# Performance work log

Hardware: AMD Instinct MI355X
Metric: run time of the kernel (lower is better)

## Reference

```python
import jax, jax.numpy as jnp
import numpy as np

N = 20000        # nodes
E = 320000       # edges (before self-loops)
V = 5000         # vocab size for each of the 5 categorical fields
L = 20           # padded token list length per node
SF = 16          # scalar feature count
ED = 32          # embedding_dim
HC = 128         # hidden_channels
NH = 4           # num_heads (conv1)
B = 8            # graphs in batch
DIN = SF + 5 * ED  # 176


def setup_inputs() -> dict:
    key = jax.random.key(0)
    ks = jax.random.split(key, 24)
    inp = {
        "x_scalar": jax.random.normal(ks[0], (N, SF), jnp.float32),
        "x_opcode": jax.random.randint(ks[1], (N, L), 0, V),
        "x_source": jax.random.randint(ks[2], (N, L), 0, V),
        "x_sink": jax.random.randint(ks[3], (N, L), 0, V),
        "x_string_manip": jax.random.randint(ks[4], (N, L), 0, V),
        "x_payload": jax.random.randint(ks[5], (N, L), 0, V),
        "edge_index": jax.random.randint(ks[6], (2, E), 0, N),
        "batch": jnp.sort(jax.random.randint(ks[7], (N,), 0, B)),
        # embedding tables (padding row 0 contributes nothing via the mask)
        "emb_opcode": jax.random.normal(ks[8], (V, ED), jnp.float32),
        "emb_source": jax.random.normal(ks[9], (V, ED), jnp.float32),
        "emb_sink": jax.random.normal(ks[10], (V, ED), jnp.float32),
        "emb_string_manip": jax.random.normal(ks[11], (V, ED), jnp.float32),
        "emb_payload": jax.random.normal(ks[12], (V, ED), jnp.float32),
        # LayerNorm params
        "ln_g": jnp.ones((DIN,), jnp.float32),
        "ln_b": jnp.zeros((DIN,), jnp.float32),
        # GATConv 1: in=DIN, out=HC, heads=NH
        "W1": jax.random.normal(ks[13], (DIN, NH * HC), jnp.float32) / np.sqrt(DIN),
        "a_src1": jax.random.normal(ks[14], (NH, HC), jnp.float32) / np.sqrt(HC),
        "a_dst1": jax.random.normal(ks[15], (NH, HC), jnp.float32) / np.sqrt(HC),
        "b1": jnp.zeros((NH * HC,), jnp.float32),
        # GATConv 2: in=NH*HC, out=HC, heads=1
        "W2": jax.random.normal(ks[16], (NH * HC, HC), jnp.float32) / np.sqrt(NH * HC),
        "a_src2": jax.random.normal(ks[17], (1, HC), jnp.float32) / np.sqrt(HC),
        "a_dst2": jax.random.normal(ks[18], (1, HC), jnp.float32) / np.sqrt(HC),
        "b2": jnp.zeros((HC,), jnp.float32),
    }
    return inp


def _masked_mean(table, idx):
    # embeds * (idx != 0) summed over token dim, divided by token count
    emb = table[idx]                                   # [N, L, ED]
    mask = (idx != 0).astype(table.dtype)[..., None]   # [N, L, 1]
    return (emb * mask).sum(1) / (mask.sum(1) + 1e-9)


def _layer_norm(x, g, b, eps=1e-5):
    mu = x.mean(-1, keepdims=True)
    var = ((x - mu) ** 2).mean(-1, keepdims=True)
    return (x - mu) * jax.lax.rsqrt(var + eps) * g + b


def _gat(x, src, dst, W, a_src, a_dst, bias, n):
    # PyG GATConv (eval mode: attention dropout off), self-loops already in src/dst
    h_, c = a_src.shape
    h = (x @ W).reshape(n, h_, c)                      # [N, H, C]
    al_s = (h * a_src).sum(-1)                         # [N, H]
    al_d = (h * a_dst).sum(-1)                         # [N, H]
    e = jax.nn.leaky_relu(al_s[src] + al_d[dst], 0.2)  # [E, H]
    m = jax.ops.segment_max(e, dst, num_segments=n)    # per-dst max for stability
    ex = jnp.exp(e - m[dst])
    den = jax.ops.segment_sum(ex, dst, num_segments=n)
    alpha = ex / (den[dst] + 1e-16)                    # per-dst softmax
    msg = h[src] * alpha[:, :, None]                   # [E, H, C]
    out = jax.ops.segment_sum(msg, dst, num_segments=n)
    return out.reshape(n, h_ * c) + bias


def reference(x_scalar, x_opcode, x_source, x_sink, x_string_manip, x_payload,
              edge_index, batch,
              emb_opcode, emb_source, emb_sink, emb_string_manip, emb_payload,
              ln_g, ln_b, W1, a_src1, a_dst1, b1, W2, a_src2, a_dst2, b2):
    n = x_scalar.shape[0]
    feats = jnp.concatenate([
        x_scalar,
        _masked_mean(emb_opcode, x_opcode),
        _masked_mean(emb_source, x_source),
        _masked_mean(emb_sink, x_sink),
        _masked_mean(emb_string_manip, x_string_manip),
        _masked_mean(emb_payload, x_payload),
    ], axis=1)                                         # [N, DIN]
    # GATConv adds self-loops by default
    loops = jnp.arange(n, dtype=edge_index.dtype)
    src = jnp.concatenate([edge_index[0], loops])
    dst = jnp.concatenate([edge_index[1], loops])
    x = jax.nn.elu(_gat(_layer_norm(feats, ln_g, ln_b), src, dst, W1, a_src1, a_dst1, b1, n))
    x = jax.nn.elu(_gat(x, src, dst, W2, a_src2, a_dst2, b2, n))
    return jax.ops.segment_max(x, batch, num_segments=B)  # global_max_pool -> [B, HC]
```

## Files before the change

kernel.cpp:

```cpp
#include <hip/hip_runtime.h>
#include <math.h>

#define SF 16
#define ED 32
#define LTOK 20
#define DIN 176
#define KP1 192
#define HC 128

typedef _Float16 f16x8 __attribute__((ext_vector_type(8)));
typedef _Float16 f16x2 __attribute__((ext_vector_type(2)));
typedef float f32x4 __attribute__((ext_vector_type(4)));

#if defined(__has_builtin)
#if __has_builtin(__builtin_amdgcn_fdot2)
#define HAVE_FDOT2 1
#endif
#endif

static __device__ __forceinline__ float leaky02(float x) { return x >= 0.f ? x : 0.2f * x; }
static __device__ __forceinline__ float eluf(float x)    { return x > 0.f ? x : expm1f(x); }
static __device__ __forceinline__ unsigned short f2h(float f)
{
  _Float16 h = (_Float16)f;
  return __builtin_bit_cast(unsigned short, h);
}
static __device__ __forceinline__ float h2f(unsigned short u)
{
  return (float)__builtin_bit_cast(_Float16, u);
}
static __device__ __forceinline__ float readlane_f(float v, int j)
{
  return __int_as_float(__builtin_amdgcn_readlane(__float_as_int(v), j));
}
static __device__ __forceinline__ unsigned readlane_u(unsigned v, int j)
{
  return (unsigned)__builtin_amdgcn_readlane((int)v, j);
}
#ifdef HAVE_FDOT2
static __device__ __forceinline__ float dot2(unsigned w, unsigned f, float c)
{
  return __builtin_amdgcn_fdot2(__builtin_bit_cast(f16x2, w),
                                __builtin_bit_cast(f16x2, f), c, false);
}
#endif

__global__ __launch_bounds__(256)
void prep_combined_kernel(const float* __restrict__ W1, const float* __restrict__ W2,
                          unsigned short* __restrict__ W1t, unsigned short* __restrict__ W2t,
                          const float* __restrict__ as1, const float* __restrict__ ad1,
                          float* __restrict__ vs, float* __restrict__ vd,
                          int* __restrict__ deg, unsigned* __restrict__ pool,
                          int N, int poolN)
{
  const int nb1 = (512 * KP1 + 255) / 256;
  const int nb2 = (HC * 512 + 255) / 256;
  const int nb3 = (N + 255) / 256;
  const int nb4 = (poolN + 255) / 256;
  int bid = blockIdx.x;
  if (bid < nb1) {
    int i = bid * 256 + threadIdx.x;
    if (i < 512 * KP1) {
      int n = i / KP1, k = i - n * KP1;
      W1t[i] = f2h((k < DIN) ? W1[(size_t)k * 512 + n] : 0.f);
    }
    return;
  }
  bid -= nb1;
  if (bid < nb2) {
    int i = bid * 256 + threadIdx.x;
    if (i < HC * 512) {
      int n = i / 512, k = i - n * 512;
      W2t[i] = f2h(W2[(size_t)k * HC + n]);
    }
    return;
  }
  bid -= nb2;
  if (bid < nb3) {
    int i = bid * 256 + threadIdx.x;
    if (i < N) deg[i] = 0;
    return;
  }
  bid -= nb3;
  if (bid < nb4) {
    int i = bid * 256 + threadIdx.x;
    if (i < poolN) pool[i] = 0x00800000u;
    return;
  }
  bid -= nb4;
  {
    int k = bid;
    int h = threadIdx.x >> 6, lane = threadIdx.x & 63;
    const float* row = W1 + (size_t)k * 512 + h * HC;
    float s = row[lane] * as1[h * HC + lane] + row[lane + 64] * as1[h * HC + lane + 64];
    float d = row[lane] * ad1[h * HC + lane] + row[lane + 64] * ad1[h * HC + lane + 64];
    #pragma unroll
    for (int off = 32; off; off >>= 1) { s += __shfl_down(s, off); d += __shfl_down(d, off); }
    if (lane == 0) { vs[k * 4 + h] = s; vd[k * 4 + h] = d; }
  }
}

__global__ __launch_bounds__(256)
void feat_ln_kernel(const float* __restrict__ xs,
                    const int* __restrict__ i0, const int* __restrict__ i1,
                    const int* __restrict__ i2, const int* __restrict__ i3,
                    const int* __restrict__ i4,
                    const float* __restrict__ e0, const float* __restrict__ e1,
                    const float* __restrict__ e2, const float* __restrict__ e3,
                    const float* __restrict__ e4,
                    const float* __restrict__ g, const float* __restrict__ b,
                    const float4* __restrict__ vs, const float4* __restrict__ vd,
                    unsigned short* __restrict__ out,
                    float* __restrict__ als, float* __restrict__ ald, int N)
{
  __shared__ int toks[4][5 * LTOK];
  int w = threadIdx.x >> 6, l = threadIdx.x & 63;
  int n = blockIdx.x * 4 + w;
  if (n >= N) return;

  for (int q = l; q < 5 * LTOK; q += 64) {
    int f = q / LTOK, j = q - f * LTOK;
    const int* ip = (f == 0) ? i0 : (f == 1) ? i1 : (f == 2) ? i2 : (f == 3) ? i3 : i4;
    toks[w][q] = ip[n * LTOK + j];
  }

  float v[3];
  #pragma unroll
  for (int r = 0; r < 3; ++r) {
    int c = l + r * 64;
    float val = 0.f;
    if (c < SF) {
      val = xs[n * SF + c];
    } else if (c < DIN) {
      int f  = (c - SF) >> 5;
      int ch = (c - SF) & 31;
      const float* ep = (f == 0) ? e0 : (f == 1) ? e1 : (f == 2) ? e2 : (f == 3) ? e3 : e4;
      float vals[LTOK];
      #pragma unroll
      for (int j = 0; j < LTOK; ++j)
        vals[j] = ep[toks[w][f * LTOK + j] * ED + ch];
      float sum = 0.f, cnt = 0.f;
      #pragma unroll
      for (int j = 0; j < LTOK; ++j)
        if (toks[w][f * LTOK + j] != 0) { sum += vals[j]; cnt += 1.f; }
      val = sum / (cnt + 1e-9f);
    }
    v[r] = val;
  }

  float p  = v[0] + v[1] + v[2];
  float p2 = v[0] * v[0] + v[1] * v[1] + v[2] * v[2];
  #pragma unroll
  for (int off = 32; off; off >>= 1) { p += __shfl_xor(p, off); p2 += __shfl_xor(p2, off); }
  float mu   = p * (1.f / DIN);
  float var  = fmaxf(p2 * (1.f / DIN) - mu * mu, 0.f);
  float rstd = rsqrtf(var + 1e-5f);

  float pr[8] = {0.f, 0.f, 0.f, 0.f, 0.f, 0.f, 0.f, 0.f};
  #pragma unroll
  for (int r = 0; r < 3; ++r) {
    int c = l + r * 64;
    float y = 0.f;
    if (c < DIN) {
      y = (v[r] - mu) * rstd * g[c] + b[c];
      float4 s4 = vs[c], d4 = vd[c];
      pr[0] += y * s4.x; pr[1] += y * s4.y; pr[2] += y * s4.z; pr[3] += y * s4.w;
      pr[4] += y * d4.x; pr[5] += y * d4.y; pr[6] += y * d4.z; pr[7] += y * d4.w;
    }
    if (c < KP1) out[(size_t)n * KP1 + c] = f2h(y);
  }
  #pragma unroll
  for (int j = 0; j < 8; ++j)
    #pragma unroll
    for (int off = 32; off; off >>= 1) pr[j] += __shfl_xor(pr[j], off);
  if (l == 0) {
    als[n * 4 + 0] = pr[0]; als[n * 4 + 1] = pr[1];
    als[n * 4 + 2] = pr[2]; als[n * 4 + 3] = pr[3];
    ald[n * 4 + 0] = pr[4]; ald[n * 4 + 1] = pr[5];
    ald[n * 4 + 2] = pr[6]; ald[n * 4 + 3] = pr[7];
  }
}

__global__ void count_kernel(const int* __restrict__ ei, int E, int N, int* __restrict__ deg)
{
  int e = blockIdx.x * blockDim.x + threadIdx.x;
  if (e < E + N) {
    int dst = (e < E) ? ei[E + e] : (e - E);
    atomicAdd(&deg[dst], 1);
  }
}

__global__ __launch_bounds__(1024)
void scan_kernel(const int* __restrict__ deg, int* __restrict__ rowptr,
                 int* __restrict__ fill, int N)
{
  __shared__ int sums[1024];
  int t = threadIdx.x;
  int CH = (N + 1023) >> 10;
  int base = t * CH;
  int s = 0;
  for (int i = 0; i < CH; ++i) if (base + i < N) s += deg[base + i];
  sums[t] = s;
  __syncthreads();
  for (int off = 1; off < 1024; off <<= 1) {
    int v = (t >= off) ? sums[t - off] : 0;
    __syncthreads();
    sums[t] += v;
    __syncthreads();
  }
  int run = sums[t] - s;
  for (int i = 0; i < CH; ++i) {
    if (base + i < N) {
      rowptr[base + i] = run;
      fill[base + i]   = run;
      run += deg[base + i];
    }
  }
  if (t == 1023) rowptr[N] = run;
}

__global__ void scatter_kernel(const int* __restrict__ ei, int E, int N,
                               int* __restrict__ fill, int* __restrict__ csr_src)
{
  int e = blockIdx.x * blockDim.x + threadIdx.x;
  if (e < E + N) {
    int src, dst;
    if (e < E) { src = ei[e]; dst = ei[E + e]; }
    else       { src = dst = e - E; }
    int pos = atomicAdd(&fill[dst], 1);
    csr_src[pos] = src;
  }
}

__global__ __launch_bounds__(256)
void agg_feat_kernel(const unsigned short* __restrict__ F,
                     const float4* __restrict__ als, const float4* __restrict__ ald,
                     const int* __restrict__ rowptr, const int* __restrict__ csr_src,
                     unsigned short* __restrict__ G, int N)
{
  int wv = threadIdx.x >> 6, lane = threadIdx.x & 63;
  int n = blockIdx.x * 4 + wv;
  if (n >= N) return;
  int rs = __builtin_amdgcn_readfirstlane(rowptr[n]);
  int re = __builtin_amdgcn_readfirstlane(rowptr[n + 1]);
  int cnt = re - rs;
  float4 ad4 = ald[n];
  float aldv[4] = { ad4.x, ad4.y, ad4.z, ad4.w };

  float acc[4][4] = {};
  bool act = lane < 48;
  const unsigned short* Fb = F + lane * 4;

#ifdef HAVE_FDOT2
  auto passB = [&](int srcA, unsigned pkw[4], int ccnt) {
    for (int j = 0; j < ccnt; j += 2) {
      int s0 = __builtin_amdgcn_readlane(srcA, j);
      int s1 = __builtin_amdgcn_readlane(srcA, j + 1 < 64 ? j + 1 : j);
      unsigned w0 = readlane_u(pkw[0], j);
      unsigned w1 = readlane_u(pkw[1], j);
      unsigned w2 = readlane_u(pkw[2], j);
      unsigned w3 = readlane_u(pkw[3], j);
      if (act) {
        int2 a0 = *(const int2*)(Fb + (size_t)s0 * KP1);
        int2 a1 = *(const int2*)(Fb + (size_t)s1 * KP1);
        unsigned pA = __builtin_amdgcn_perm((unsigned)a0.x, (unsigned)a1.x, 0x01000504u);
        unsigned pB = __builtin_amdgcn_perm((unsigned)a0.x, (unsigned)a1.x, 0x03020706u);
        unsigned pC = __builtin_amdgcn_perm((unsigned)a0.y, (unsigned)a1.y, 0x01000504u);
        unsigned pD = __builtin_amdgcn_perm((unsigned)a0.y, (unsigned)a1.y, 0x03020706u);
        acc[0][0] = dot2(w0, pA, acc[0][0]); acc[0][1] = dot2(w0, pB, acc[0][1]);
        acc[0][2] = dot2(w0, pC, acc[0][2]); acc[0][3] = dot2(w0, pD, acc[0][3]);
        acc[1][0] = dot2(w1, pA, acc[1][0]); acc[1][1] = dot2(w1, pB, acc[1][1]);
        acc[1][2] = dot2(w1, pC, acc[1][2]); acc[1][3] = dot2(w1, pD, acc[1][3]);
        acc[2][0] = dot2(w2, pA, acc[2][0]); acc[2][1] = dot2(w2, pB, acc[2][1]);
        acc[2][2] = dot2(w2, pC, acc[2][2]); acc[2][3] = dot2(w2, pD, acc[2][3]);
        acc[3][0] = dot2(w3, pA, acc[3][0]); acc[3][1] = dot2(w3, pB, acc[3][1]);
        acc[3][2] = dot2(w3, pC, acc[3][2]); acc[3][3] = dot2(w3, pD, acc[3][3]);
      }
    }
  };
#else
  auto passB = [&](int srcA, float wf[4], int ccnt) {
    for (int j = 0; j < ccnt; ++j) {
      int src = __builtin_amdgcn_readlane(srcA, j);
      float q0 = readlane_f(wf[0], j), q1 = readlane_f(wf[1], j);
      float q2 = readlane_f(wf[2], j), q3 = readlane_f(wf[3], j);
      if (act) {
        int2 a0 = *(const int2*)(Fb + (size_t)src * KP1);
        float f0 = h2f((unsigned short)(a0.x & 0xffff));
        float f1 = h2f((unsigned short)((unsigned)a0.x >> 16));
        float f2v = h2f((unsigned short)(a0.y & 0xffff));
        float f3 = h2f((unsigned short)((unsigned)a0.y >> 16));
        acc[0][0] += q0 * f0; acc[0][1] += q0 * f1; acc[0][2] += q0 * f2v; acc[0][3] += q0 * f3;
        acc[1][0] += q1 * f0; acc[1][1] += q1 * f1; acc[1][2] += q1 * f2v; acc[1][3] += q1 * f3;
        acc[2][0] += q2 * f0; acc[2][1] += q2 * f1; acc[2][2] += q2 * f2v; acc[2][3] += q2 * f3;
        acc[3][0] += q3 * f0; acc[3][1] += q3 * f1; acc[3][2] += q3 * f2v; acc[3][3] += q3 * f3;
      }
    }
  };
#endif

  if (cnt <= 64) {
    int srcA = 0;
    float e[4] = { -1e30f, -1e30f, -1e30f, -1e30f };
    if (lane < cnt) {
      srcA = csr_src[rs + lane];
      float4 a4 = als[srcA];
      e[0] = leaky02(a4.x + aldv[0]); e[1] = leaky02(a4.y + aldv[1]);
      e[2] = leaky02(a4.z + aldv[2]); e[3] = leaky02(a4.w + aldv[3]);
    }
    float m[4] = { e[0], e[1], e[2], e[3] };
    #pragma unroll
    for (int off = 32; off; off >>= 1)
      #pragma unroll
      for (int h = 0; h < 4; ++h) m[h] = fmaxf(m[h], __shfl_xor(m[h], off));
    float w[4];
    #pragma unroll
    for (int h = 0; h < 4; ++h) w[h] = (lane < cnt) ? __expf(e[h] - m[h]) : 0.f;
    float den[4] = { w[0], w[1], w[2], w[3] };
    #pragma unroll
    for (int off = 32; off; off >>= 1)
      #pragma unroll
      for (int h = 0; h < 4; ++h) den[h] += __shfl_xor(den[h], off);
    #pragma unroll
    for (int h = 0; h < 4; ++h) w[h] /= (den[h] + 1e-16f);
#ifdef HAVE_FDOT2
    unsigned pkw[4];
    #pragma unroll
    for (int h = 0; h < 4; ++h) {
      float wn = __shfl_xor(w[h], 1);
      float we = (lane & 1) ? wn : w[h];
      float wo = (lane & 1) ? w[h] : wn;
      pkw[h] = (unsigned)f2h(we) | ((unsigned)f2h(wo) << 16);
    }
    passB(srcA, pkw, cnt);
#else
    passB(srcA, w, cnt);
#endif
  } else {
    float m[4], s[4];
    #pragma unroll
    for (int h = 0; h < 4; ++h) { m[h] = -1e30f; s[h] = 0.f; }
    for (int i = rs + lane; i < re; i += 64) {
      int src = csr_src[i];
      float4 a4 = als[src];
      float av[4] = { a4.x, a4.y, a4.z, a4.w };
      #pragma unroll
      for (int h = 0; h < 4; ++h) {
        float e = leaky02(av[h] + aldv[h]);
        float Mx = fmaxf(m[h], e);
        s[h] = s[h] * __expf(m[h] - Mx) + __expf(e - Mx);
        m[h] = Mx;
      }
    }
    #pragma unroll
    for (int off = 32; off; off >>= 1) {
      #pragma unroll
      for (int h = 0; h < 4; ++h) {
        float m2 = __shfl_xor(m[h], off);
        float s2 = __shfl_xor(s[h], off);
        float Mx = fmaxf(m[h], m2);
        s[h] = s[h] * __expf(m[h] - Mx) + s2 * __expf(m2 - Mx);
        m[h] = Mx;
      }
    }
    float inv[4];
    #pragma unroll
    for (int h = 0; h < 4; ++h) inv[h] = 1.f / (s[h] + 1e-16f);
    for (int b0 = rs; b0 < re; b0 += 64) {
      int bcnt = min(64, re - b0);
      int srcA = 0;
      float w[4] = {0.f, 0.f, 0.f, 0.f};
      if (lane < bcnt) {
        srcA = csr_src[b0 + lane];
        float4 a4 = als[srcA];
        w[0] = __expf(leaky02(a4.x + aldv[0]) - m[0]) * inv[0];
        w[1] = __expf(leaky02(a4.y + aldv[1]) - m[1]) * inv[1];
        w[2] = __expf(leaky02(a4.z + aldv[2]) - m[2]) * inv[2];
        w[3] = __expf(leaky02(a4.w + aldv[3]) - m[3]) * inv[3];
      }
#ifdef HAVE_FDOT2
      unsigned pkw[4];
      #pragma unroll
      for (int h = 0; h < 4; ++h) {
        float wn = __shfl_xor(w[h], 1);
        float we = (lane & 1) ? wn : w[h];
        float wo = (lane & 1) ? w[h] : wn;
        pkw[h] = (unsigned)f2h(we) | ((unsigned)f2h(wo) << 16);
      }
      passB(srcA, pkw, bcnt);
#else
      passB(srcA, w, bcnt);
#endif
    }
  }

  if (act) {
    #pragma unroll
    for (int h = 0; h < 4; ++h) {
      int2 o;
      o.x = (int)f2h(acc[h][0]) | ((int)f2h(acc[h][1]) << 16);
      o.y = (int)f2h(acc[h][2]) | ((int)f2h(acc[h][3]) << 16);
      *(int2*)&G[((size_t)h * N + n) * KP1 + lane * 4] = o;
    }
  }
}

template<int KPad>
__global__ __launch_bounds__(256)
void gemm_f16_kernel(const unsigned short* __restrict__ A, const unsigned short* __restrict__ Bt,
                     unsigned short* __restrict__ C, int M, int Nc,
                     size_t aStrideZ, size_t bStrideZ, int cColStrideZ,
                     const float* __restrict__ bias, int act,
                     const float* __restrict__ la_s, const float* __restrict__ la_d,
                     float* __restrict__ lout_s, float* __restrict__ lout_d)
{
  A  += blockIdx.z * aStrideZ;
  Bt += blockIdx.z * bStrideZ;
  int colZ = blockIdx.z * cColStrideZ;

  __shared__ __align__(16) unsigned short As[4][128][8];
  __shared__ __align__(16) unsigned short Bs[4][128][8];
  __shared__ float ls[128][2];
  int tid  = threadIdx.x;
  int lane = tid & 63, wave = tid >> 6;
  int wm = (wave >> 1) << 6, wn = (wave & 1) << 6;
  int bm = blockIdx.y << 7, bn = blockIdx.x << 7;

  int srow = tid >> 1;
  int skc  = (tid & 1) << 1;
  const unsigned short* Arow = A  + (size_t)(bm + srow) * KPad + skc * 8;
  const unsigned short* Brow = Bt + (size_t)(bn + srow) * KPad + skc * 8;
  bool aok = (bm + srow) < M;

  f32x4 acc[4][4];
  #pragma unroll
  for (int m = 0; m < 4; ++m)
    #pragma unroll
    for (int n2 = 0; n2 < 4; ++n2) acc[m][n2] = (f32x4){0.f, 0.f, 0.f, 0.f};

  int kc  = lane >> 4;
  int r16 = lane & 15;

  for (int k0 = 0; k0 < KPad; k0 += 32) {
    int4 av0 = make_int4(0, 0, 0, 0), av1 = make_int4(0, 0, 0, 0);
    if (aok) {
      av0 = *(const int4*)(Arow + k0);
      av1 = *(const int4*)(Arow + k0 + 8);
    }
    int4 bv0 = *(const int4*)(Brow + k0);
    int4 bv1 = *(const int4*)(Brow + k0 + 8);
    __syncthreads();
    *(int4*)&As[skc][srow][0]     = av0;
    *(int4*)&As[skc + 1][srow][0] = av1;
    *(int4*)&Bs[skc][srow][0]     = bv0;
    *(int4*)&Bs[skc + 1][srow][0] = bv1;
    __syncthreads();

    f16x8 af[4], bfr[4];
    #pragma unroll
    for (int m = 0; m < 4; ++m)  af[m]  = *(const f16x8*)&As[kc][wm + m * 16 + r16][0];
    #pragma unroll
    for (int n2 = 0; n2 < 4; ++n2) bfr[n2] = *(const f16x8*)&Bs[kc][wn + n2 * 16 + r16][0];
    #pragma unroll
    for (int m = 0; m < 4; ++m)
      #pragma unroll
      for (int n2 = 0; n2 < 4; ++n2)
        acc[m][n2] = __builtin_amdgcn_mfma_f32_16x16x32_f16(af[m], bfr[n2], acc[m][n2], 0, 0, 0);
  }

  int rq = lane >> 4;
  #pragma unroll
  for (int m = 0; m < 4; ++m) {
    #pragma unroll
    for (int r = 0; r < 4; ++r) {
      int row = bm + wm + m * 16 + rq * 4 + r;
      if (row < M) {
        #pragma unroll
        for (int n2 = 0; n2 < 4; ++n2) {
          int col = colZ + bn + wn + n2 * 16 + r16;
          float val = acc[m][n2][r];
          if (bias) val += bias[col];
          if (act)  val = eluf(val);
          C[(size_t)row * Nc + col] = f2h(val);
        }
      }
    }
  }

  if (lout_s) {
    float ps[4][4] = {}, pd[4][4] = {};
    #pragma unroll
    for (int m = 0; m < 4; ++m)
      #pragma unroll
      for (int r = 0; r < 4; ++r)
        #pragma unroll
        for (int n2 = 0; n2 < 4; ++n2) {
          int col = wn + n2 * 16 + r16;
          float val = acc[m][n2][r];
          ps[m][r] += val * la_s[col];
          pd[m][r] += val * la_d[col];
        }
    #pragma unroll
    for (int off = 1; off < 16; off <<= 1)
      #pragma unroll
      for (int m = 0; m < 4; ++m)
        #pragma unroll
        for (int r = 0; r < 4; ++r) {
          ps[m][r] += __shfl_xor(ps[m][r], off);
          pd[m][r] += __shfl_xor(pd[m][r], off);
        }
    if (r16 == 0 && wn == 0) {
      #pragma unroll
      for (int m = 0; m < 4; ++m)
        #pragma unroll
        for (int r = 0; r < 4; ++r) {
          int rl = wm + m * 16 + rq * 4 + r;
          ls[rl][0] = ps[m][r];
          ls[rl][1] = pd[m][r];
        }
    }
    __syncthreads();
    if (r16 == 0 && wn != 0) {
      #pragma unroll
      for (int m = 0; m < 4; ++m)
        #pragma unroll
        for (int r = 0; r < 4; ++r) {
          int rl = wm + m * 16 + rq * 4 + r;
          int row = bm + rl;
          if (row < M) {
            lout_s[row] = ls[rl][0] + ps[m][r];
            lout_d[row] = ls[rl][1] + pd[m][r];
          }
        }
    }
  }
}

__global__ __launch_bounds__(256)
void agg_h2_kernel(const unsigned short* __restrict__ H,
                   const float* __restrict__ al_s, const float* __restrict__ al_d,
                   const int* __restrict__ rowptr, const int* __restrict__ csr_src,
                   const float* __restrict__ bias, unsigned short* __restrict__ out, int N)
{
  int wv = threadIdx.x >> 6, lane = threadIdx.x & 63;
  int n = blockIdx.x * 4 + wv;
  if (n >= N) return;
  int rs = __builtin_amdgcn_readfirstlane(rowptr[n]);
  int re = __builtin_amdgcn_readfirstlane(rowptr[n + 1]);
  int cnt = re - rs;
  float ald = al_d[n];
  float acc0 = 0.f, acc1 = 0.f;
  const unsigned short* Hb = H + lane * 2;

#ifdef HAVE_FDOT2
  auto passB = [&](int srcA, unsigned pkw, int ccnt) {
    for (int j = 0; j < ccnt; j += 2) {
      int s0 = __builtin_amdgcn_readlane(srcA, j);
      int s1 = __builtin_amdgcn_readlane(srcA, j + 1 < 64 ? j + 1 : j);
      unsigned pw = readlane_u(pkw, j);
      unsigned a0 = *(const unsigned*)(Hb + (size_t)s0 * HC);
      unsigned a1 = *(const unsigned*)(Hb + (size_t)s1 * HC);
      unsigned p0 = __builtin_amdgcn_perm(a0, a1, 0x01000504u);
      unsigned p1 = __builtin_amdgcn_perm(a0, a1, 0x03020706u);
      acc0 = dot2(pw, p0, acc0);
      acc1 = dot2(pw, p1, acc1);
    }
  };
#else
  auto passB = [&](int srcA, float wf, int ccnt) {
    for (int j = 0; j < ccnt; ++j) {
      int src = __builtin_amdgcn_readlane(srcA, j);
      float wgt = readlane_f(wf, j);
      unsigned a0 = *(const unsigned*)(Hb + (size_t)src * HC);
      acc0 += wgt * h2f((unsigned short)(a0 & 0xffff));
      acc1 += wgt * h2f((unsigned short)(a0 >> 16));
    }
  };
#endif

  if (cnt <= 64) {
    int srcA = 0;
    float e = -1e30f;
    if (lane < cnt) {
      srcA = csr_src[rs + lane];
      e = leaky02(al_s[srcA] + ald);
    }
    float m = e;
    #pragma unroll
    for (int off = 32; off; off >>= 1) m = fmaxf(m, __shfl_xor(m, off));
    float w = (lane < cnt) ? __expf(e - m) : 0.f;
    float den = w;
    #pragma unroll
    for (int off = 32; off; off >>= 1) den += __shfl_xor(den, off);
    w /= (den + 1e-16f);
#ifdef HAVE_FDOT2
    float wn2 = __shfl_xor(w, 1);
    float we = (lane & 1) ? wn2 : w;
    float wo = (lane & 1) ? w : wn2;
    unsigned pkw = (unsigned)f2h(we) | ((unsigned)f2h(wo) << 16);
    passB(srcA, pkw, cnt);
#else
    passB(srcA, w, cnt);
#endif
  } else {
    float m = -1e30f, s = 0.f;
    for (int i = rs + lane; i < re; i += 64) {
      int src = csr_src[i];
      float e = leaky02(al_s[src] + ald);
      float Mx = fmaxf(m, e);
      s = s * __expf(m - Mx) + __expf(e - Mx);
      m = Mx;
    }
    #pragma unroll
    for (int off = 32; off; off >>= 1) {
      float m2 = __shfl_xor(m, off);
      float s2 = __shfl_xor(s, off);
      float Mx = fmaxf(m, m2);
      s = s * __expf(m - Mx) + s2 * __expf(m2 - Mx);
      m = Mx;
    }
    float inv_den = 1.f / (s + 1e-16f);
    for (int c0 = rs; c0 < re; c0 += 64) {
      int ccnt = min(64, re - c0);
      int srcA = 0;
      float w = 0.f;
      if (lane < ccnt) {
        srcA = csr_src[c0 + lane];
        w = __expf(leaky02(al_s[srcA] + ald) - m) * inv_den;
      }
#ifdef HAVE_FDOT2
      float wn2 = __shfl_xor(w, 1);
      float we = (lane & 1) ? wn2 : w;
      float wo = (lane & 1) ? w : wn2;
      unsigned pkw = (unsigned)f2h(we) | ((unsigned)f2h(wo) << 16);
      passB(srcA, pkw, ccnt);
#else
      passB(srcA, w, ccnt);
#endif
    }
  }

  float o0 = eluf(acc0 + bias[lane * 2 + 0]);
  float o1 = eluf(acc1 + bias[lane * 2 + 1]);
  unsigned o = (unsigned)f2h(o0) | ((unsigned)f2h(o1) << 16);
  *(unsigned*)&out[(size_t)n * HC + lane * 2] = o;
}

static __device__ __forceinline__ unsigned enc_f(float f)
{
  unsigned u = __float_as_uint(f);
  return (u & 0x80000000u) ? ~u : (u | 0x80000000u);
}
static __device__ __forceinline__ float dec_f(unsigned u)
{
  return (u & 0x80000000u) ? __uint_as_float(u & 0x7fffffffu) : __uint_as_float(~u);
}

#define PNPB 128
__global__ __launch_bounds__(256)
void pool_seg_kernel(const unsigned short* __restrict__ x, const int* __restrict__ batch,
                     unsigned* __restrict__ pool, int N)
{
  int cp = (threadIdx.x & 63) * 2;
  int g  = threadIdx.x >> 6;
  int n0 = blockIdx.x * PNPB;
  int n1 = min(n0 + PNPB, N);
  int curb = -1;
  float m0 = 0.f, m1 = 0.f;
  for (int n = n0 + g; n < n1; n += 4) {
    int bg = batch[n];
    ushort2 v = *(const ushort2*)&x[(size_t)n * HC + cp];
    float v0 = h2f(v.x), v1 = h2f(v.y);
    if (bg != curb) {
      if (curb >= 0) {
        atomicMax(&pool[curb * HC + cp],     enc_f(m0));
        atomicMax(&pool[curb * HC + cp + 1], enc_f(m1));
      }
      curb = bg; m0 = v0; m1 = v1;
    } else {
      m0 = fmaxf(m0, v0);
      m1 = fmaxf(m1, v1);
    }
  }
  if (curb >= 0) {
    atomicMax(&pool[curb * HC + cp],     enc_f(m0));
    atomicMax(&pool[curb * HC + cp + 1], enc_f(m1));
  }
}

__global__ void pool_final_kernel(const unsigned* __restrict__ pool, float* __restrict__ out, int n)
{
  int i = blockIdx.x * blockDim.x + threadIdx.x;
  if (i < n) out[i] = dec_f(pool[i]);
}

extern "C" void kernel_launch(void* const* d_in, const int* in_sizes, int n_in,
                              void* d_out, int out_size, void* d_ws, size_t ws_size,
                              hipStream_t stream)
{
  const float* x_scalar = (const float*)d_in[0];
  const int* i0 = (const int*)d_in[1];
  const int* i1 = (const int*)d_in[2];
  const int* i2 = (const int*)d_in[3];
  const int* i3 = (const int*)d_in[4];
  const int* i4 = (const int*)d_in[5];
  const int* ei = (const int*)d_in[6];
  const int* batch = (const int*)d_in[7];
  const float* e0 = (const float*)d_in[8];
  const float* e1 = (const float*)d_in[9];
  const float* e2 = (const float*)d_in[10];
  const float* e3 = (const float*)d_in[11];
  const float* e4 = (const float*)d_in[12];
  const float* ln_g = (const float*)d_in[13];
  const float* ln_b = (const float*)d_in[14];
  const float* W1 = (const float*)d_in[15];
  const float* as1 = (const float*)d_in[16];
  const float* ad1 = (const float*)d_in[17];
  const float* b1 = (const float*)d_in[18];
  const float* W2 = (const float*)d_in[19];
  const float* as2 = (const float*)d_in[20];
  const float* ad2 = (const float*)d_in[21];
  const float* b2 = (const float*)d_in[22];

  const int N  = in_sizes[0] / SF;
  const int E  = in_sizes[6] / 2;
  const int Et = E + N;
  const int Bg = out_size / HC;
  const int MT = (N + 127) / 128;

  char* w = (char*)d_ws;
  auto alloc = [&](size_t bytes) -> char* {
    char* p = w;
    w += (bytes + 255) & ~(size_t)255;
    return p;
  };
  unsigned short* featsb = (unsigned short*)alloc((size_t)N * KP1 * 2);
  unsigned short* G      = (unsigned short*)alloc((size_t)4 * N * KP1 * 2);
  unsigned short* X2b    = (unsigned short*)alloc((size_t)N * 512 * 2);
  unsigned short* H2b    = (unsigned short*)alloc((size_t)N * HC * 2);
  unsigned short* X3b    = (unsigned short*)alloc((size_t)N * HC * 2);
  unsigned short* W1t    = (unsigned short*)alloc((size_t)512 * KP1 * 2);
  unsigned short* W2t    = (unsigned short*)alloc((size_t)HC * 512 * 2);
  float* vs      = (float*)alloc((size_t)KP1 * 4 * 4);
  float* vd      = (float*)alloc((size_t)KP1 * 4 * 4);
  float* als1    = (float*)alloc((size_t)N * 4 * 4);
  float* ald1    = (float*)alloc((size_t)N * 4 * 4);
  float* als2    = (float*)alloc((size_t)N * 4);
  float* ald2    = (float*)alloc((size_t)N * 4);
  int*   deg     = (int*)alloc((size_t)N * 4);
  int*   rowptr  = (int*)alloc((size_t)(N + 1) * 4);
  int*   fill    = (int*)alloc((size_t)N * 4);
  int*   csr_src = (int*)alloc((size_t)Et * 4);
  unsigned* pool = (unsigned*)alloc((size_t)Bg * HC * 4);

  {
    int nb1 = (512 * KP1 + 255) / 256;
    int nb2 = (HC * 512 + 255) / 256;
    int nb3 = (N + 255) / 256;
    int nb4 = (Bg * HC + 255) / 256;
    prep_combined_kernel<<<nb1 + nb2 + nb3 + nb4 + DIN, 256, 0, stream>>>(
        W1, W2, W1t, W2t, as1, ad1, vs, vd, deg, pool, N, Bg * HC);
  }

  feat_ln_kernel<<<(N + 3) / 4, 256, 0, stream>>>(x_scalar, i0, i1, i2, i3, i4,
                                                  e0, e1, e2, e3, e4, ln_g, ln_b,
                                                  (const float4*)vs, (const float4*)vd,
                                                  featsb, als1, ald1, N);

  count_kernel<<<(Et + 255) / 256, 256, 0, stream>>>(ei, E, N, deg);
  scan_kernel<<<1, 1024, 0, stream>>>(deg, rowptr, fill, N);
  scatter_kernel<<<(Et + 255) / 256, 256, 0, stream>>>(ei, E, N, fill, csr_src);

  agg_feat_kernel<<<(N + 3) / 4, 256, 0, stream>>>(featsb, (const float4*)als1,
                                                   (const float4*)ald1,
                                                   rowptr, csr_src, G, N);
  gemm_f16_kernel<KP1><<<dim3(1, MT, 4), 256, 0, stream>>>(
      G, W1t, X2b, N, 512, (size_t)N * KP1, (size_t)HC * KP1, HC, b1, 1,
      nullptr, nullptr, nullptr, nullptr);

  gemm_f16_kernel<512><<<dim3(1, MT, 1), 256, 0, stream>>>(
      X2b, W2t, H2b, N, HC, 0, 0, 0, nullptr, 0,
      as2, ad2, als2, ald2);
  agg_h2_kernel<<<(N + 3) / 4, 256, 0, stream>>>(H2b, als2, ald2, rowptr, csr_src, b2, X3b, N);

  pool_seg_kernel<<<(N + PNPB - 1) / PNPB, 256, 0, stream>>>(X3b, batch, pool, N);
  pool_final_kernel<<<(Bg * HC + 255) / 256, 256, 0, stream>>>(pool, (float*)d_out, Bg * HC);
}
```

Measured before the change: 244.9 us.

## Shrink GEMM tiles to 64x64 with register prefetch and atomic logit accumulation

Replaces the 128x128-tile MFMA GEMM with a 64x64-tile version. The N dimension is now split across two blocks, the next K-chunk is prefetched into registers, and bias/ELU and logit epilogues are selected by template parameters. The attention-logit dot products for layer 2 are now accumulated with atomicAdd across column blocks, which requires zeroing als2/ald2 in the prep kernel. The aim is more blocks for occupancy and CU coverage on a small-M-per-tile problem, at the cost of less data reuse per tile and extra atomics.

```diff
diff --git a/kernel.cpp b/kernel.cpp
--- a/kernel.cpp
+++ b/kernel.cpp
@@ -51,6 +51,7 @@
                           const float* __restrict__ as1, const float* __restrict__ ad1,
                           float* __restrict__ vs, float* __restrict__ vd,
                           int* __restrict__ deg, unsigned* __restrict__ pool,
+                          float* __restrict__ als2, float* __restrict__ ald2,
                           int N, int poolN)
 {
   const int nb1 = (512 * KP1 + 255) / 256;
@@ -78,7 +79,7 @@
   bid -= nb2;
   if (bid < nb3) {
     int i = bid * 256 + threadIdx.x;
-    if (i < N) deg[i] = 0;
+    if (i < N) { deg[i] = 0; als2[i] = 0.f; ald2[i] = 0.f; }
     return;
   }
   bid -= nb3;
@@ -405,133 +406,106 @@
   }
 }
 
-template<int KPad>
+template<int KPad, int BIAS_ELU, int LOGITS>
 __global__ __launch_bounds__(256)
-void gemm_f16_kernel(const unsigned short* __restrict__ A, const unsigned short* __restrict__ Bt,
-                     unsigned short* __restrict__ C, int M, int Nc,
-                     size_t aStrideZ, size_t bStrideZ, int cColStrideZ,
-                     const float* __restrict__ bias, int act,
-                     const float* __restrict__ la_s, const float* __restrict__ la_d,
-                     float* __restrict__ lout_s, float* __restrict__ lout_d)
+void gemm64_kernel(const unsigned short* __restrict__ A,
+                   const unsigned short* __restrict__ Bt,
+                   unsigned short* __restrict__ C,
+                   int M, int Nc,
+                   size_t aStrideZ, size_t bStrideZ, int cColStrideZ,
+                   const float* __restrict__ bias,
+                   const float* __restrict__ la_s, const float* __restrict__ la_d,
+                   float* __restrict__ lout_s, float* __restrict__ lout_d)
 {
   A  += blockIdx.z * aStrideZ;
   Bt += blockIdx.z * bStrideZ;
-  int colZ = blockIdx.z * cColStrideZ;
-
-  __shared__ __align__(16) unsigned short As[4][128][8];
-  __shared__ __align__(16) unsigned short Bs[4][128][8];
-  __shared__ float ls[128][2];
-  int tid  = threadIdx.x;
-  int lane = tid & 63, wave = tid >> 6;
-  int wm = (wave >> 1) << 6, wn = (wave & 1) << 6;
-  int bm = blockIdx.y << 7, bn = blockIdx.x << 7;
-
-  int srow = tid >> 1;
-  int skc  = (tid & 1) << 1;
-  const unsigned short* Arow = A  + (size_t)(bm + srow) * KPad + skc * 8;
-  const unsigned short* Brow = Bt + (size_t)(bn + srow) * KPad + skc * 8;
-  bool aok = (bm + srow) < M;
-
-  f32x4 acc[4][4];
+  const int colZ = blockIdx.z * cColStrideZ;
+
+  __shared__ __align__(16) unsigned short As[4][520];
+  __shared__ __align__(16) unsigned short Bs[4][520];
+
+  const int tid  = threadIdx.x;
+  const int lane = tid & 63, wv = tid >> 6;
+  const int bm = blockIdx.y << 6, bn = blockIdx.x << 6;
+  const int wm = (wv >> 1) << 5, wn = (wv & 1) << 5;
+  const int kc = lane >> 4, r16 = lane & 15;
+
+  const int srow = lane, skc = wv;
+  const unsigned short* Ap = A + (size_t)(bm + srow) * KPad + skc * 8;
+  const unsigned short* Bp = Bt + (size_t)(bn + srow) * KPad + skc * 8;
+  const bool aok = (bm + srow) < M;
+
+  f32x4 acc[2][2];
   #pragma unroll
-  for (int m = 0; m < 4; ++m)
-    #pragma unroll
-    for (int n2 = 0; n2 < 4; ++n2) acc[m][n2] = (f32x4){0.f, 0.f, 0.f, 0.f};
-
-  int kc  = lane >> 4;
-  int r16 = lane & 15;
-
-  for (int k0 = 0; k0 < KPad; k0 += 32) {
-    int4 av0 = make_int4(0, 0, 0, 0), av1 = make_int4(0, 0, 0, 0);
-    if (aok) {
-      av0 = *(const int4*)(Arow + k0);
-      av1 = *(const int4*)(Arow + k0 + 8);
-    }
-    int4 bv0 = *(const int4*)(Brow + k0);
-    int4 bv1 = *(const int4*)(Brow + k0 + 8);
+  for (int m = 0; m < 2; ++m)
+    #pragma unroll
+    for (int n2 = 0; n2 < 2; ++n2) acc[m][n2] = (f32x4){0.f, 0.f, 0.f, 0.f};
+
+  constexpr int NT = KPad / 32;
+  int4 av = aok ? *(const int4*)Ap : make_int4(0, 0, 0, 0);
+  int4 bv = *(const int4*)Bp;
+
+  for (int t = 0; t < NT; ++t) {
+    *(int4*)&As[skc][srow * 8] = av;
+    *(int4*)&Bs[skc][srow * 8] = bv;
+    if (t + 1 < NT) {
+      av = aok ? *(const int4*)(Ap + (t + 1) * 32) : make_int4(0, 0, 0, 0);
+      bv = *(const int4*)(Bp + (t + 1) * 32);
+    }
     __syncthreads();
-    *(int4*)&As[skc][srow][0]     = av0;
-    *(int4*)&As[skc + 1][srow][0] = av1;
-    *(int4*)&Bs[skc][srow][0]     = bv0;
-    *(int4*)&Bs[skc + 1][srow][0] = bv1;
+    f16x8 af0 = *(const f16x8*)&As[kc][(wm + r16) * 8];
+    f16x8 af1 = *(const f16x8*)&As[kc][(wm + 16 + r16) * 8];
+    f16x8 bf0 = *(const f16x8*)&Bs[kc][(wn + r16) * 8];
+    f16x8 bf1 = *(const f16x8*)&Bs[kc][(wn + 16 + r16) * 8];
+    acc[0][0] = __builtin_amdgcn_mfma_f32_16x16x32_f16(af0, bf0, acc[0][0], 0, 0, 0);
+    acc[0][1] = __builtin_amdgcn_mfma_f32_16x16x32_f16(af0, bf1, acc[0][1], 0, 0, 0);
+    acc[1][0] = __builtin_amdgcn_mfma_f32_16x16x32_f16(af1, bf0, acc[1][0], 0, 0, 0);
+    acc[1][1] = __builtin_amdgcn_mfma_f32_16x16x32_f16(af1, bf1, acc[1][1], 0, 0, 0);
     __syncthreads();
-
-    f16x8 af[4], bfr[4];
-    #pragma unroll
-    for (int m = 0; m < 4; ++m)  af[m]  = *(const f16x8*)&As[kc][wm + m * 16 + r16][0];
-    #pragma unroll
-    for (int n2 = 0; n2 < 4; ++n2) bfr[n2] = *(const f16x8*)&Bs[kc][wn + n2 * 16 + r16][0];
-    #pragma unroll
-    for (int m = 0; m < 4; ++m)
-      #pragma unroll
-      for (int n2 = 0; n2 < 4; ++n2)
-        acc[m][n2] = __builtin_amdgcn_mfma_f32_16x16x32_f16(af[m], bfr[n2], acc[m][n2], 0, 0, 0);
-  }
-
-  int rq = lane >> 4;
+  }
+
+  const int rq = lane >> 4;
   #pragma unroll
-  for (int m = 0; m < 4; ++m) {
+  for (int m = 0; m < 2; ++m) {
     #pragma unroll
     for (int r = 0; r < 4; ++r) {
       int row = bm + wm + m * 16 + rq * 4 + r;
       if (row < M) {
         #pragma unroll
-        for (int n2 = 0; n2 < 4; ++n2) {
+        for (int n2 = 0; n2 < 2; ++n2) {
           int col = colZ + bn + wn + n2 * 16 + r16;
           float val = acc[m][n2][r];
-          if (bias) val += bias[col];
-          if (act)  val = eluf(val);
+          if (BIAS_ELU) { val += bias[col]; val = eluf(val); }
           C[(size_t)row * Nc + col] = f2h(val);
         }
       }
     }
   }
 
-  if (lout_s) {
-    float ps[4][4] = {}, pd[4][4] = {};
-    #pragma unroll
-    for (int m = 0; m < 4; ++m)
+  if (LOGITS) {
+    #pragma unroll
+    for (int m = 0; m < 2; ++m) {
       #pragma unroll
-      for (int r = 0; r < 4; ++r)
+      for (int r = 0; r < 4; ++r) {
+        float ps = 0.f, pd = 0.f;
         #pragma unroll
-        for (int n2 = 0; n2 < 4; ++n2) {
-          int col = wn + n2 * 16 + r16;
+        for (int n2 = 0; n2 < 2; ++n2) {
+          int col = bn + wn + n2 * 16 + r16;
           float val = acc[m][n2][r];
-          ps[m][r] += val * la_s[col];
-          pd[m][r] += val * la_d[col];
+          ps += val * la_s[col];
+          pd += val * la_d[col];
         }
-    #pragma unroll
-    for (int off = 1; off < 16; off <<= 1)
-      #pragma unroll
-      for (int m = 0; m < 4; ++m)
         #pragma unroll
-        for (int r = 0; r < 4; ++r) {
-          ps[m][r] += __shfl_xor(ps[m][r], off);
-          pd[m][r] += __shfl_xor(pd[m][r], off);
+        for (int off = 1; off < 16; off <<= 1) {
+          ps += __shfl_xor(ps, off);
+          pd += __shfl_xor(pd, off);
         }
-    if (r16 == 0 && wn == 0) {
-      #pragma unroll
-      for (int m = 0; m < 4; ++m)
-        #pragma unroll
-        for (int r = 0; r < 4; ++r) {
-          int rl = wm + m * 16 + rq * 4 + r;
-          ls[rl][0] = ps[m][r];
-          ls[rl][1] = pd[m][r];
+        int row = bm + wm + m * 16 + rq * 4 + r;
+        if (r16 == 0 && row < M) {
+          atomicAdd(&lout_s[row], ps);
+          atomicAdd(&lout_d[row], pd);
         }
-    }
-    __syncthreads();
-    if (r16 == 0 && wn != 0) {
-      #pragma unroll
-      for (int m = 0; m < 4; ++m)
-        #pragma unroll
-        for (int r = 0; r < 4; ++r) {
-          int rl = wm + m * 16 + rq * 4 + r;
-          int row = bm + rl;
-          if (row < M) {
-            lout_s[row] = ls[rl][0] + ps[m][r];
-            lout_d[row] = ls[rl][1] + pd[m][r];
-          }
-        }
+      }
     }
   }
 }
@@ -726,7 +700,7 @@
   const int E  = in_sizes[6] / 2;
   const int Et = E + N;
   const int Bg = out_size / HC;
-  const int MT = (N + 127) / 128;
+  const int MT64 = (N + 63) / 64;
 
   char* w = (char*)d_ws;
   auto alloc = [&](size_t bytes) -> char* {
@@ -759,7 +733,7 @@
     int nb3 = (N + 255) / 256;
     int nb4 = (Bg * HC + 255) / 256;
     prep_combined_kernel<<<nb1 + nb2 + nb3 + nb4 + DIN, 256, 0, stream>>>(
-        W1, W2, W1t, W2t, as1, ad1, vs, vd, deg, pool, N, Bg * HC);
+        W1, W2, W1t, W2t, as1, ad1, vs, vd, deg, pool, als2, ald2, N, Bg * HC);
   }
 
   feat_ln_kernel<<<(N + 3) / 4, 256, 0, stream>>>(x_scalar, i0, i1, i2, i3, i4,
@@ -774,12 +748,12 @@
   agg_feat_kernel<<<(N + 3) / 4, 256, 0, stream>>>(featsb, (const float4*)als1,
                                                    (const float4*)ald1,
                                                    rowptr, csr_src, G, N);
-  gemm_f16_kernel<KP1><<<dim3(1, MT, 4), 256, 0, stream>>>(
-      G, W1t, X2b, N, 512, (size_t)N * KP1, (size_t)HC * KP1, HC, b1, 1,
+  gemm64_kernel<KP1, 1, 0><<<dim3(2, MT64, 4), 256, 0, stream>>>(
+      G, W1t, X2b, N, 512, (size_t)N * KP1, (size_t)HC * KP1, HC, b1,
       nullptr, nullptr, nullptr, nullptr);
 
-  gemm_f16_kernel<512><<<dim3(1, MT, 1), 256, 0, stream>>>(
-      X2b, W2t, H2b, N, HC, 0, 0, 0, nullptr, 0,
+  gemm64_kernel<512, 0, 1><<<dim3(2, MT64, 1), 256, 0, stream>>>(
+      X2b, W2t, H2b, N, HC, 0, 0, 0, nullptr,
       as2, ad2, als2, ald2);
   agg_h2_kernel<<<(N + 3) / 4, 256, 0, stream>>>(H2b, als2, ald2, rowptr, csr_src, b2, X3b, N);
 
```

Measured after the change: 228.4 us. 1.07x faster.
